# Optimization experiments

Hardware: AMD Instinct MI355X
Metric: run time of the kernel (lower is better)

The kernel has to match this reference:

```python
import jax, jax.numpy as jnp
import numpy as np
from jax import lax

FEAT = 56  # features_size
SR = 2     # sr_ratio
NUM_HEADS = 8

# Constant relative-distance indices, shape (N, N, 2) with values in [0, 2*FEAT-2]
_idx = np.array([[i, j] for i in range(FEAT) for j in range(FEAT)])
REL = jnp.asarray(_idx[None, :, :] - _idx[:, None, :] + FEAT - 1)  # (N, N, 2)


def setup_inputs() -> dict:
    key = jax.random.key(0)
    ks = jax.random.split(key, 8)
    dim = 256
    B = 4
    x = jax.random.normal(ks[0], (B, dim, FEAT, FEAT), dtype=jnp.float32)
    Wq = jax.random.normal(ks[1], (dim, dim), dtype=jnp.float32) * 0.02
    Wkv = jax.random.normal(ks[2], (dim, 2 * dim), dtype=jnp.float32) * 0.02
    sr_w = jax.random.normal(ks[3], (dim, dim, SR, SR), dtype=jnp.float32) * 0.02  # OIHW
    sr_b = jnp.zeros((dim,), dtype=jnp.float32)
    ln_g = jnp.ones((dim,), dtype=jnp.float32)
    ln_b = jnp.zeros((dim,), dtype=jnp.float32)
    pos_emb = jax.random.normal(ks[4], (2 * FEAT - 1, 2 * FEAT - 1), dtype=jnp.float32) * 0.2
    proj_w = jax.random.normal(ks[5], (dim, dim), dtype=jnp.float32) * 0.02
    proj_b = jnp.zeros((dim,), dtype=jnp.float32)
    return {"x": x, "Wq": Wq, "Wkv": Wkv, "sr_w": sr_w, "sr_b": sr_b,
            "ln_g": ln_g, "ln_b": ln_b, "pos_emb": pos_emb,
            "proj_w": proj_w, "proj_b": proj_b}


def reference(x, Wq, Wkv, sr_w, sr_b, ln_g, ln_b, pos_emb, proj_w, proj_b):
    B, C, H, W = x.shape
    N = H * W
    h = NUM_HEADS
    hd = C // h
    scale = hd ** -0.5

    x_q = x.reshape(B, C, N).transpose(0, 2, 1)            # (B, N, C)
    q = (x_q @ Wq).reshape(B, N, h, hd).transpose(0, 2, 1, 3)  # (B, h, N, hd)

    # spatial reduction conv (kernel=stride=SR) + layernorm
    xr = lax.conv_general_dilated(x, sr_w, (SR, SR), 'VALID',
                                  dimension_numbers=('NCHW', 'OIHW', 'NCHW'))
    xr = xr + sr_b[None, :, None, None]
    Nk = (H // SR) * (W // SR)
    x_kv = xr.reshape(B, C, Nk).transpose(0, 2, 1)          # (B, Nk, C)
    mu = jnp.mean(x_kv, axis=-1, keepdims=True)
    var = jnp.var(x_kv, axis=-1, keepdims=True)
    x_kv = (x_kv - mu) * lax.rsqrt(var + 1e-5) * ln_g + ln_b

    # kv projection; einops '(dim h l)' split: head_dim slowest, l fastest
    kv = (x_kv @ Wkv).reshape(B, Nk, hd, h, 2)
    k = kv[..., 0].transpose(0, 3, 1, 2)                    # (B, h, Nk, hd)
    v = kv[..., 1].transpose(0, 3, 1, 2)                    # (B, h, Nk, hd)

    attn = jnp.einsum('bhnd,bhmd->bhnm', q, k) * scale      # (B, h, N, Nk)
    bias = pos_emb[REL[..., 0], REL[..., 1]][:, :Nk]        # (N, Nk)
    attn = jax.nn.softmax(attn + bias, axis=-1)

    out = jnp.einsum('bhnm,bhmd->bhnd', attn, v)            # (B, h, N, hd)
    out = out.transpose(0, 2, 1, 3).reshape(B, N, C)
    out = out @ proj_w + proj_b
    return out.transpose(0, 2, 1).reshape(B, C, H, W)
```

## Files before the change

kernel.cpp:

```cpp
#include <hip/hip_runtime.h>
#include <hip/hip_bf16.h>

typedef float f32x4 __attribute__((ext_vector_type(4)));
typedef short s16x8 __attribute__((ext_vector_type(8)));
typedef unsigned short u16x8 __attribute__((ext_vector_type(8)));

#define MFMA16(a,b,c) __builtin_amdgcn_mfma_f32_16x16x32_bf16(a,b,c,0,0,0)

#define NTOK 3136
#define NKV  784
#define NKVP 800
#define CD   256
#define NH   8
#define HD   32
#define PEW  111
#define LOG2E 1.4426950408889634f
#define SC2  (0.17677669529663687f * 1.4426950408889634f)

static __device__ __forceinline__ unsigned short f2b(float f){
  unsigned int u = __float_as_uint(f);
  return (unsigned short)((u + 0x7fffu + ((u>>16)&1u)) >> 16);
}
static __device__ __forceinline__ unsigned short f2b_fast(float f){
  __hip_bfloat16 h = __float2bfloat16(f);
  return *reinterpret_cast<unsigned short*>(&h);
}
static __device__ __forceinline__ float b2f(unsigned short u){
  return __uint_as_float(((unsigned int)u)<<16);
}

__global__ void k_prepw(const float* __restrict__ Wq, const float* __restrict__ Wkv,
                        const float* __restrict__ pw, const float* __restrict__ srw,
                        unsigned short* __restrict__ WqT, unsigned short* __restrict__ WkvT,
                        unsigned short* __restrict__ pwT, unsigned short* __restrict__ srwb2){
  int i = blockIdx.x*256 + threadIdx.x;
  if (i < 65536){ int nn=i>>8, kk=i&255; WqT[i] = f2b(Wq[kk*256+nn]); }
  else if (i < 196608){ int j=i-65536; int c2=j>>8, kk=j&255; WkvT[j] = f2b(Wkv[kk*512+c2]); }
  else if (i < 262144){ int j=i-196608; int cc=j>>8, kk=j&255; pwT[j] = f2b(pw[kk*256+cc]); }
  else { int j=i-262144; int o=j>>10, rem=j&1023, khw=rem>>8, ci=rem&255;
         srwb2[j] = f2b(srw[o*1024 + ci*4 + khw]); }
}

__global__ void k_bias(const float* __restrict__ pos, unsigned short* __restrict__ bias2){
  int key = blockIdx.x*256 + threadIdx.x;
  int n = blockIdx.y;
  if (key >= NKVP) return;
  float v;
  if (key < NKV){
    int nr = (n*9363)>>19, nc = n - nr*56;
    int tt = (key*9363)>>19, mm = key - tt*56;
    v = pos[(tt-nr+55)*PEW + (mm-nc+55)] * LOG2E;
  } else v = -100000.f;
  bias2[(size_t)n*NKVP + key] = f2b(v);
}

__global__ void k_pad(unsigned short* __restrict__ kb, unsigned short* __restrict__ vT){
  int i = blockIdx.x*256 + threadIdx.x;
  if (i < 16384){
    int bh=i>>9, r=i&511, ridx=r>>5, d=r&31;
    int row = 776 + (ridx&7) + (ridx>>3)*16;
    kb[((size_t)bh*NKVP + row)*HD + d] = 0;
  } else {
    int j=i-16384;
    int bh=j>>9, r=j&511, d=r>>4, key=784+(r&15);
    vT[((size_t)bh*HD + d)*NKVP + key] = 0;
  }
}

__global__ __launch_bounds__(256) void k_xt(const float* __restrict__ x,
                                            unsigned short* __restrict__ xbf){
  __shared__ float tile[64][65];
  const int t = threadIdx.x;
  const int n0 = blockIdx.x*64, c0 = blockIdx.y*64, b = blockIdx.z;
  const int tx = t&15, ty = t>>4;
#pragma unroll
  for (int j=0;j<4;++j){
    f32x4 v = *(const f32x4*)&x[(size_t)(b*CD + c0+ty+j*16)*NTOK + n0 + tx*4];
    tile[ty+j*16][tx*4+0]=v[0]; tile[ty+j*16][tx*4+1]=v[1];
    tile[ty+j*16][tx*4+2]=v[2]; tile[ty+j*16][tx*4+3]=v[3];
  }
  __syncthreads();
  const int nr = t>>2, ccb = (t&3)*16;
  u16x8 o0, o1;
#pragma unroll
  for (int u=0;u<8;++u){ o0[u] = f2b(tile[ccb+u][nr]); o1[u] = f2b(tile[ccb+8+u][nr]); }
  unsigned short* dst = &xbf[((size_t)b*NTOK + n0+nr)*CD + c0 + ccb];
  *(u16x8*)dst = o0;
  *(u16x8*)(dst+8) = o1;
}

__global__ __launch_bounds__(256) void k_qproj(const unsigned short* __restrict__ xbf,
      const unsigned short* __restrict__ WqT, unsigned short* __restrict__ qb){
  const int tid=threadIdx.x, wv=tid>>6, l=tid&63, g=l>>4, ln16=l&15;
  const int bI = blockIdx.x/49;
  const int n0 = (blockIdx.x%49)*64;
  const int m0 = n0 + (wv>>1)*32;
  const int c0 = blockIdx.y*64 + (wv&1)*32;
  const unsigned short* ap0 = &xbf[((size_t)bI*NTOK + m0+ln16)*CD + g*8];
  const unsigned short* ap1 = ap0 + 16*CD;
  const unsigned short* bp0 = &WqT[(size_t)(c0+ln16)*CD + g*8];
  const unsigned short* bp1 = bp0 + 16*CD;
  f32x4 acc[2][2] = {};
  s16x8 a0 = *(const s16x8*)ap0, a1 = *(const s16x8*)ap1;
  s16x8 w0 = *(const s16x8*)bp0, w1 = *(const s16x8*)bp1;
#pragma unroll
  for (int k0=0; k0<CD; k0+=32){
    s16x8 na0 = *(const s16x8*)(ap0 + k0+32);
    s16x8 na1 = *(const s16x8*)(ap1 + k0+32);
    s16x8 nw0 = *(const s16x8*)(bp0 + k0+32);
    s16x8 nw1 = *(const s16x8*)(bp1 + k0+32);
    acc[0][0] = MFMA16(a0, w0, acc[0][0]);
    acc[0][1] = MFMA16(a0, w1, acc[0][1]);
    acc[1][0] = MFMA16(a1, w0, acc[1][0]);
    acc[1][1] = MFMA16(a1, w1, acc[1][1]);
    a0=na0; a1=na1; w0=nw0; w1=nw1;
  }
#pragma unroll
  for (int mi=0;mi<2;++mi)
#pragma unroll
    for (int ni=0;ni<2;++ni){
      int c = c0 + ni*16 + ln16;
#pragma unroll
      for (int r=0;r<4;++r){
        int n = m0 + mi*16 + g*4 + r;
        qb[((size_t)bI*NTOK + n)*CD + c] = f2b(acc[mi][ni][r] * SC2);
      }
    }
}

__global__ __launch_bounds__(256) void k_conv(const unsigned short* __restrict__ xbf,
      const unsigned short* __restrict__ srwb2, const float* __restrict__ srb,
      float* __restrict__ convo){
  const int tid=threadIdx.x, wv=tid>>6, l=tid&63, g=l>>4, ln16=l&15;
  const int m0 = blockIdx.x*64 + (wv>>1)*32;
  const int c0 = blockIdx.y*64 + (wv&1)*32;
  size_t abase[2][4];
#pragma unroll
  for (int mi=0;mi<2;++mi){
    int m = m0 + mi*16 + ln16;
    int bb = (m>=2352)?3:(m>=1568)?2:(m>=784)?1:0;
    int nk = m - bb*784;
    int pp = (nk*9363)>>18, qq = nk - pp*28;
#pragma unroll
    for (int khw=0;khw<4;++khw){
      int kh = khw>>1, kw = khw&1;
      abase[mi][khw] = ((size_t)bb*NTOK + (2*pp+kh)*56 + 2*qq+kw)*CD;
    }
  }
  const unsigned short* wp0 = &srwb2[(size_t)(c0+ln16)*1024 + g*8];
  const unsigned short* wp1 = wp0 + 16*1024;
  f32x4 acc[2][2] = {};
  s16x8 a0 = *(const s16x8*)&xbf[abase[0][0] + g*8];
  s16x8 a1 = *(const s16x8*)&xbf[abase[1][0] + g*8];
  s16x8 w0 = *(const s16x8*)wp0;
  s16x8 w1 = *(const s16x8*)wp1;
#pragma unroll
  for (int s=0; s<32; ++s){
    const int s1 = s+1;
    const int khw2 = (s1>>3)&3, kc2 = (s1&7)*32;
    const int woff = (s1&31)*32;
    s16x8 na0 = *(const s16x8*)&xbf[abase[0][khw2] + kc2 + g*8];
    s16x8 na1 = *(const s16x8*)&xbf[abase[1][khw2] + kc2 + g*8];
    s16x8 nw0 = *(const s16x8*)(wp0 + woff);
    s16x8 nw1 = *(const s16x8*)(wp1 + woff);
    acc[0][0] = MFMA16(a0, w0, acc[0][0]);
    acc[0][1] = MFMA16(a0, w1, acc[0][1]);
    acc[1][0] = MFMA16(a1, w0, acc[1][0]);
    acc[1][1] = MFMA16(a1, w1, acc[1][1]);
    a0=na0; a1=na1; w0=nw0; w1=nw1;
  }
#pragma unroll
  for (int mi=0;mi<2;++mi)
#pragma unroll
    for (int ni=0;ni<2;++ni){
      int c = c0 + ni*16 + ln16;
      float bias = srb[c];
#pragma unroll
      for (int r=0;r<4;++r){
        int m = m0 + mi*16 + g*4 + r;
        convo[(size_t)m*CD + c] = acc[mi][ni][r] + bias;
      }
    }
}

__global__ void k_ln(const float* __restrict__ co, const float* __restrict__ gam,
                     const float* __restrict__ bet, unsigned short* __restrict__ kvbf){
  const int row = blockIdx.x, t = threadIdx.x;
  float v = co[(size_t)row*CD + t];
  float s = v, s2 = v*v;
#pragma unroll
  for (int o=32; o>0; o>>=1){ s += __shfl_down(s,o); s2 += __shfl_down(s2,o); }
  __shared__ float ps[4], ps2[4];
  int wid = t>>6, lane = t&63;
  if (lane==0){ ps[wid]=s; ps2[wid]=s2; }
  __syncthreads();
  if (t==0){
    float a = ps[0]+ps[1]+ps[2]+ps[3];
    float a2 = ps2[0]+ps2[1]+ps2[2]+ps2[3];
    float mu = a*(1.f/CD);
    float var = a2*(1.f/CD) - mu*mu;
    ps[0] = mu; ps2[0] = rsqrtf(var + 1e-5f);
  }
  __syncthreads();
  float mu = ps[0], rs = ps2[0];
  kvbf[(size_t)row*CD + t] = f2b((v-mu)*rs*gam[t] + bet[t]);
}

__global__ __launch_bounds__(256) void k_kv(const unsigned short* __restrict__ kvbf,
      const unsigned short* __restrict__ WkvT, unsigned short* __restrict__ kb,
      unsigned short* __restrict__ vT){
  const int tid=threadIdx.x, wv=tid>>6, l=tid&63, g=l>>4, ln16=l&15;
  const int m0 = blockIdx.x*64 + (wv>>1)*32;
  const int c0 = blockIdx.y*64 + (wv&1)*32;
  const unsigned short* ap0 = &kvbf[(size_t)(m0+ln16)*CD + g*8];
  const unsigned short* ap1 = ap0 + 16*CD;
  const unsigned short* bp0 = &WkvT[(size_t)(c0+ln16)*CD + g*8];
  const unsigned short* bp1 = bp0 + 16*CD;
  f32x4 acc[2][2] = {};
  s16x8 a0 = *(const s16x8*)ap0, a1 = *(const s16x8*)ap1;
  s16x8 w0 = *(const s16x8*)bp0, w1 = *(const s16x8*)bp1;
#pragma unroll
  for (int k0=0; k0<CD; k0+=32){
    s16x8 na0 = *(const s16x8*)(ap0 + k0+32);
    s16x8 na1 = *(const s16x8*)(ap1 + k0+32);
    s16x8 nw0 = *(const s16x8*)(bp0 + k0+32);
    s16x8 nw1 = *(const s16x8*)(bp1 + k0+32);
    acc[0][0] = MFMA16(a0, w0, acc[0][0]);
    acc[0][1] = MFMA16(a0, w1, acc[0][1]);
    acc[1][0] = MFMA16(a1, w0, acc[1][0]);
    acc[1][1] = MFMA16(a1, w1, acc[1][1]);
    a0=na0; a1=na1; w0=nw0; w1=nw1;
  }
#pragma unroll
  for (int mi=0;mi<2;++mi)
#pragma unroll
    for (int ni=0;ni<2;++ni){
      int c2 = c0 + ni*16 + ln16;
      int d = c2>>4, hh = (c2>>1)&7;
#pragma unroll
      for (int r=0;r<4;++r){
        int m = m0 + mi*16 + g*4 + r;
        int bq = (m>=2352)?3:(m>=1568)?2:(m>=784)?1:0;
        int nk = m - bq*784;
        unsigned short val = f2b(acc[mi][ni][r]);
        if (c2&1){
          vT[(((size_t)bq*NH+hh)*HD + d)*NKVP + nk] = val;
        } else {
          int chunk = nk & ~31, pos = nk & 31;
          int gg = pos>>3, jj = pos&7;
          int row = (jj<4) ? (gg*4+jj) : (16 + gg*4 + (jj-4));
          kb[(((size_t)bq*NH+hh)*NKVP + chunk + row)*HD + d] = val;
        }
      }
    }
}

__global__ __launch_bounds__(256) void k_attn(const unsigned short* __restrict__ qb,
      const unsigned short* __restrict__ kb, const unsigned short* __restrict__ vT,
      const unsigned short* __restrict__ bias2, unsigned short* __restrict__ aout){
  const int tid=threadIdx.x, wv=tid>>6, l=tid&63, g=l>>4, ln16=l&15;
  const int bh = blockIdx.y, b = bh>>3, h = bh&7;
  const int nw = blockIdx.x*64 + wv*16;
  const s16x8 qf = *(const s16x8*)&qb[((size_t)b*NTOK + nw + ln16)*CD + h*HD + g*8];
  const unsigned short* kptr  = kb + (size_t)bh*NKVP*HD + ln16*HD + g*8;
  const unsigned short* vptr0 = vT + (size_t)bh*HD*NKVP + ln16*NKVP + g*8;
  const unsigned short* vptr1 = vptr0 + 16*NKVP;
  const unsigned short* bp = bias2 + (size_t)(nw + ln16)*NKVP + g*8;
  f32x4 accO0 = {}, accO1 = {};
  float S = 0.f;
  const f32x4 zf = {};
  s16x8 ka0 = *(const s16x8*)(kptr);
  s16x8 ka1 = *(const s16x8*)(kptr + 16*HD);
  s16x8 v0  = *(const s16x8*)(vptr0);
  s16x8 v1  = *(const s16x8*)(vptr1);
  u16x8 bb  = *(const u16x8*)(bp);
#pragma unroll 5
  for (int it=0; it<25; ++it){
    kptr += 32*HD; vptr0 += 32; vptr1 += 32; bp += 32;
    s16x8 nk0 = *(const s16x8*)(kptr);
    s16x8 nk1 = *(const s16x8*)(kptr + 16*HD);
    s16x8 nv0 = *(const s16x8*)(vptr0);
    s16x8 nv1 = *(const s16x8*)(vptr1);
    u16x8 nbb = *(const u16x8*)(bp);
    f32x4 d0 = MFMA16(ka0, qf, zf);
    f32x4 d1 = MFMA16(ka1, qf, zf);
    float p[8];
#pragma unroll
    for (int r=0;r<4;++r){
      p[r]   = exp2f(d0[r] + b2f(bb[r]));
      p[4+r] = exp2f(d1[r] + b2f(bb[4+r]));
    }
    S += ((p[0]+p[1])+(p[2]+p[3])) + ((p[4]+p[5])+(p[6]+p[7]));
    s16x8 pf;
#pragma unroll
    for (int j=0;j<8;++j) pf[j] = (short)f2b_fast(p[j]);
    accO0 = MFMA16(pf, v0, accO0);
    accO1 = MFMA16(pf, v1, accO1);
    ka0=nk0; ka1=nk1; v0=nv0; v1=nv1; bb=nbb;
  }
  S += __shfl_xor(S, 16);
  S += __shfl_xor(S, 32);
#pragma unroll
  for (int r=0;r<4;++r){
    float Sr = __shfl(S, g*4 + r);
    float inv = 1.f / Sr;
    int n = nw + g*4 + r;
    aout[((size_t)b*NTOK + n)*CD + h*HD + ln16]      = f2b(accO0[r]*inv);
    aout[((size_t)b*NTOK + n)*CD + h*HD + 16 + ln16] = f2b(accO1[r]*inv);
  }
}

__global__ __launch_bounds__(256) void k_proj(const unsigned short* __restrict__ ain,
      const unsigned short* __restrict__ pwT, const float* __restrict__ pb,
      float* __restrict__ out){
  const int tid=threadIdx.x, wv=tid>>6, l=tid&63, g=l>>4, ln16=l&15;
  const int bI = blockIdx.x/49;
  const int n0 = (blockIdx.x%49)*64;
  const int nsub = n0 + (wv&1)*32;
  const int c0 = blockIdx.y*64 + (wv>>1)*32;
  const unsigned short* ap0 = &pwT[(size_t)(c0+ln16)*CD + g*8];
  const unsigned short* ap1 = ap0 + 16*CD;
  const unsigned short* bp0 = &ain[((size_t)bI*NTOK + nsub+ln16)*CD + g*8];
  const unsigned short* bp1 = bp0 + 16*CD;
  f32x4 acc[2][2] = {};
  s16x8 a0 = *(const s16x8*)ap0, a1 = *(const s16x8*)ap1;
  s16x8 w0 = *(const s16x8*)bp0, w1 = *(const s16x8*)bp1;
#pragma unroll
  for (int k0=0; k0<CD; k0+=32){
    s16x8 na0 = *(const s16x8*)(ap0 + k0+32);
    s16x8 na1 = *(const s16x8*)(ap1 + k0+32);
    s16x8 nw0 = *(const s16x8*)(bp0 + k0+32);
    s16x8 nw1 = *(const s16x8*)(bp1 + k0+32);
    acc[0][0] = MFMA16(a0, w0, acc[0][0]);
    acc[0][1] = MFMA16(a0, w1, acc[0][1]);
    acc[1][0] = MFMA16(a1, w0, acc[1][0]);
    acc[1][1] = MFMA16(a1, w1, acc[1][1]);
    a0=na0; a1=na1; w0=nw0; w1=nw1;
  }
#pragma unroll
  for (int mi=0;mi<2;++mi)
#pragma unroll
    for (int r=0;r<4;++r){
      int c = c0 + mi*16 + g*4 + r;
      float bias = pb[c];
#pragma unroll
      for (int ni=0;ni<2;++ni){
        int n = nsub + ni*16 + ln16;
        out[((size_t)bI*CD + c)*NTOK + n] = acc[mi][ni][r] + bias;
      }
    }
}

extern "C" void kernel_launch(void* const* d_in, const int* in_sizes, int n_in,
                              void* d_out, int out_size, void* d_ws, size_t ws_size,
                              hipStream_t stream){
  const float* x   = (const float*)d_in[0];
  const float* Wq  = (const float*)d_in[1];
  const float* Wkv = (const float*)d_in[2];
  const float* srw = (const float*)d_in[3];
  const float* srb = (const float*)d_in[4];
  const float* lng = (const float*)d_in[5];
  const float* lnb = (const float*)d_in[6];
  const float* pos = (const float*)d_in[7];
  const float* pw  = (const float*)d_in[8];
  const float* pb  = (const float*)d_in[9];
  float* out = (float*)d_out;

  unsigned char* p = (unsigned char*)d_ws;
  unsigned short* WqT   = (unsigned short*)(p + 0);
  unsigned short* WkvT  = (unsigned short*)(p + 131072);
  unsigned short* pwT   = (unsigned short*)(p + 393216);
  unsigned short* srwb2 = (unsigned short*)(p + 524288);
  unsigned short* bias2 = (unsigned short*)(p + 1048576);
  unsigned short* xbf   = (unsigned short*)(p + 6066176);
  unsigned short* qbuf  = (unsigned short*)(p + 12488704);
  float*          convo = (float*)        (p + 18911232);
  unsigned short* kvbf  = (unsigned short*)(p + 22122496);
  unsigned short* kbuf  = (unsigned short*)(p + 23728128);
  unsigned short* vT    = (unsigned short*)(p + 25366528);
  unsigned short* aout  = (unsigned short*)(p + 27004928);

  k_prepw<<<2048, 256, 0, stream>>>(Wq, Wkv, pw, srw, WqT, WkvT, pwT, srwb2);
  k_bias <<<dim3(4,3136), 256, 0, stream>>>(pos, bias2);
  k_pad  <<<128, 256, 0, stream>>>(kbuf, vT);
  k_xt   <<<dim3(49,4,4), 256, 0, stream>>>(x, xbf);
  k_qproj<<<dim3(196,4), 256, 0, stream>>>(xbf, WqT, qbuf);
  k_conv <<<dim3(49,4),  256, 0, stream>>>(xbf, srwb2, srb, convo);
  k_ln   <<<3136, 256, 0, stream>>>(convo, lng, lnb, kvbf);
  k_kv   <<<dim3(49,8),  256, 0, stream>>>(kvbf, WkvT, kbuf, vT);
  k_attn <<<dim3(49,32), 256, 0, stream>>>(qbuf, kbuf, vT, bias2, aout);
  k_proj <<<dim3(196,4), 256, 0, stream>>>(aout, pwT, pb, out);
}
```

Baseline: 220.1 us.

## Stage K/V tiles through LDS with async loads and merge prep kernels

The four preprocessing kernels (weight transpose, bias table, padding, x transpose) are merged into one launch, and the bias table is now written as 4-element vectors per thread. The attention kernel now has the whole block share K and V tiles: they are loaded once per block into double-buffered LDS with global_load_lds, instead of each wave loading its own copy from global memory. The grid is also swapped so blocks of the same batch-head run next to each other, which should improve L2 reuse. This cuts redundant global K/V traffic and launch overhead, but adds a __syncthreads per iteration and an LDS read stage.

```diff
diff --git a/kernel.cpp b/kernel.cpp
--- a/kernel.cpp
+++ b/kernel.cpp
@@ -3,6 +3,7 @@
 
 typedef float f32x4 __attribute__((ext_vector_type(4)));
 typedef short s16x8 __attribute__((ext_vector_type(8)));
+typedef unsigned short u16x4 __attribute__((ext_vector_type(4)));
 typedef unsigned short u16x8 __attribute__((ext_vector_type(8)));
 
 #define MFMA16(a,b,c) __builtin_amdgcn_mfma_f32_16x16x32_bf16(a,b,c,0,0,0)
@@ -28,65 +29,77 @@
 static __device__ __forceinline__ float b2f(unsigned short u){
   return __uint_as_float(((unsigned int)u)<<16);
 }
-
-__global__ void k_prepw(const float* __restrict__ Wq, const float* __restrict__ Wkv,
-                        const float* __restrict__ pw, const float* __restrict__ srw,
-                        unsigned short* __restrict__ WqT, unsigned short* __restrict__ WkvT,
-                        unsigned short* __restrict__ pwT, unsigned short* __restrict__ srwb2){
-  int i = blockIdx.x*256 + threadIdx.x;
-  if (i < 65536){ int nn=i>>8, kk=i&255; WqT[i] = f2b(Wq[kk*256+nn]); }
-  else if (i < 196608){ int j=i-65536; int c2=j>>8, kk=j&255; WkvT[j] = f2b(Wkv[kk*512+c2]); }
-  else if (i < 262144){ int j=i-196608; int cc=j>>8, kk=j&255; pwT[j] = f2b(pw[kk*256+cc]); }
-  else { int j=i-262144; int o=j>>10, rem=j&1023, khw=rem>>8, ci=rem&255;
-         srwb2[j] = f2b(srw[o*1024 + ci*4 + khw]); }
-}
-
-__global__ void k_bias(const float* __restrict__ pos, unsigned short* __restrict__ bias2){
-  int key = blockIdx.x*256 + threadIdx.x;
-  int n = blockIdx.y;
-  if (key >= NKVP) return;
-  float v;
-  if (key < NKV){
-    int nr = (n*9363)>>19, nc = n - nr*56;
-    int tt = (key*9363)>>19, mm = key - tt*56;
-    v = pos[(tt-nr+55)*PEW + (mm-nc+55)] * LOG2E;
-  } else v = -100000.f;
-  bias2[(size_t)n*NKVP + key] = f2b(v);
-}
-
-__global__ void k_pad(unsigned short* __restrict__ kb, unsigned short* __restrict__ vT){
-  int i = blockIdx.x*256 + threadIdx.x;
-  if (i < 16384){
-    int bh=i>>9, r=i&511, ridx=r>>5, d=r&31;
-    int row = 776 + (ridx&7) + (ridx>>3)*16;
-    kb[((size_t)bh*NKVP + row)*HD + d] = 0;
+static __device__ __forceinline__ void gload16(const unsigned short* g, unsigned short* l){
+  __builtin_amdgcn_global_load_lds(
+      (const __attribute__((address_space(1))) unsigned int*)g,
+      (__attribute__((address_space(3))) unsigned int*)l, 16, 0, 0);
+}
+
+__global__ __launch_bounds__(256) void k_prep(
+      const float* __restrict__ Wq, const float* __restrict__ Wkv,
+      const float* __restrict__ pw, const float* __restrict__ srw,
+      const float* __restrict__ pos, const float* __restrict__ x,
+      unsigned short* __restrict__ WqT, unsigned short* __restrict__ WkvT,
+      unsigned short* __restrict__ pwT, unsigned short* __restrict__ srwb2,
+      unsigned short* __restrict__ bias2, unsigned short* __restrict__ xbf,
+      unsigned short* __restrict__ kb, unsigned short* __restrict__ vT){
+  __shared__ float tile[64][65];
+  const int blk = blockIdx.x, t = threadIdx.x;
+  if (blk < 2048){
+    int i = blk*256 + t;
+    if (i < 65536){ int nn=i>>8, kk=i&255; WqT[i] = f2b(Wq[kk*256+nn]); }
+    else if (i < 196608){ int j=i-65536; int c2=j>>8, kk=j&255; WkvT[j] = f2b(Wkv[kk*512+c2]); }
+    else if (i < 262144){ int j=i-196608; int cc=j>>8, kk=j&255; pwT[j] = f2b(pw[kk*256+cc]); }
+    else { int j=i-262144; int o=j>>10, rem=j&1023, khw=rem>>8, ci=rem&255;
+           srwb2[j] = f2b(srw[o*1024 + ci*4 + khw]); }
+  } else if (blk < 2176){
+    int i = (blk-2048)*256 + t;
+    if (i < 16384){
+      int bh=i>>9, r=i&511, ridx=r>>5, d=r&31;
+      int row = 776 + (ridx&7) + (ridx>>3)*16;
+      kb[((size_t)bh*NKVP + row)*HD + d] = 0;
+    } else {
+      int j=i-16384;
+      int bh=j>>9, r=j&511, d=r>>4, key=784+(r&15);
+      vT[((size_t)bh*HD + d)*NKVP + key] = 0;
+    }
+  } else if (blk < 5312){
+    int n = blk - 2176;
+    if (t < 200){
+      int nr = (n*9363)>>19, nc = n - nr*56;
+      u16x4 o;
+#pragma unroll
+      for (int j=0;j<4;++j){
+        int key = t*4 + j;
+        float v;
+        if (key < NKV){
+          int tt = (key*9363)>>19, mm = key - tt*56;
+          v = pos[(tt-nr+55)*PEW + (mm-nc+55)] * LOG2E;
+        } else v = -100000.f;
+        o[j] = f2b(v);
+      }
+      *(u16x4*)&bias2[(size_t)n*NKVP + t*4] = o;
+    }
   } else {
-    int j=i-16384;
-    int bh=j>>9, r=j&511, d=r>>4, key=784+(r&15);
-    vT[((size_t)bh*HD + d)*NKVP + key] = 0;
-  }
-}
-
-__global__ __launch_bounds__(256) void k_xt(const float* __restrict__ x,
-                                            unsigned short* __restrict__ xbf){
-  __shared__ float tile[64][65];
-  const int t = threadIdx.x;
-  const int n0 = blockIdx.x*64, c0 = blockIdx.y*64, b = blockIdx.z;
-  const int tx = t&15, ty = t>>4;
-#pragma unroll
-  for (int j=0;j<4;++j){
-    f32x4 v = *(const f32x4*)&x[(size_t)(b*CD + c0+ty+j*16)*NTOK + n0 + tx*4];
-    tile[ty+j*16][tx*4+0]=v[0]; tile[ty+j*16][tx*4+1]=v[1];
-    tile[ty+j*16][tx*4+2]=v[2]; tile[ty+j*16][tx*4+3]=v[3];
-  }
-  __syncthreads();
-  const int nr = t>>2, ccb = (t&3)*16;
-  u16x8 o0, o1;
-#pragma unroll
-  for (int u=0;u<8;++u){ o0[u] = f2b(tile[ccb+u][nr]); o1[u] = f2b(tile[ccb+8+u][nr]); }
-  unsigned short* dst = &xbf[((size_t)b*NTOK + n0+nr)*CD + c0 + ccb];
-  *(u16x8*)dst = o0;
-  *(u16x8*)(dst+8) = o1;
+    int bx = blk - 5312;
+    const int n0 = (bx%49)*64; int c4 = bx/49;
+    const int c0 = (c4&3)*64, b = c4>>2;
+    const int tx = t&15, ty = t>>4;
+#pragma unroll
+    for (int j=0;j<4;++j){
+      f32x4 v = *(const f32x4*)&x[(size_t)(b*CD + c0+ty+j*16)*NTOK + n0 + tx*4];
+      tile[ty+j*16][tx*4+0]=v[0]; tile[ty+j*16][tx*4+1]=v[1];
+      tile[ty+j*16][tx*4+2]=v[2]; tile[ty+j*16][tx*4+3]=v[3];
+    }
+    __syncthreads();
+    const int nr = t>>2, ccb = (t&3)*16;
+    u16x8 o0, o1;
+#pragma unroll
+    for (int u=0;u<8;++u){ o0[u] = f2b(tile[ccb+u][nr]); o1[u] = f2b(tile[ccb+8+u][nr]); }
+    unsigned short* dst = &xbf[((size_t)b*NTOK + n0+nr)*CD + c0 + ccb];
+    *(u16x8*)dst = o0;
+    *(u16x8*)(dst+8) = o1;
+  }
 }
 
 __global__ __launch_bounds__(256) void k_qproj(const unsigned short* __restrict__ xbf,
@@ -258,30 +271,39 @@
 __global__ __launch_bounds__(256) void k_attn(const unsigned short* __restrict__ qb,
       const unsigned short* __restrict__ kb, const unsigned short* __restrict__ vT,
       const unsigned short* __restrict__ bias2, unsigned short* __restrict__ aout){
+  __shared__ unsigned short kv[2][2048];
   const int tid=threadIdx.x, wv=tid>>6, l=tid&63, g=l>>4, ln16=l&15;
-  const int bh = blockIdx.y, b = bh>>3, h = bh&7;
-  const int nw = blockIdx.x*64 + wv*16;
+  const int bh = blockIdx.x, b = bh>>3, h = bh&7;
+  const int nw = blockIdx.y*64 + wv*16;
   const s16x8 qf = *(const s16x8*)&qb[((size_t)b*NTOK + nw + ln16)*CD + h*HD + g*8];
-  const unsigned short* kptr  = kb + (size_t)bh*NKVP*HD + ln16*HD + g*8;
-  const unsigned short* vptr0 = vT + (size_t)bh*HD*NKVP + ln16*NKVP + g*8;
-  const unsigned short* vptr1 = vptr0 + 16*NKVP;
+  const unsigned short* kbase = kb + (size_t)bh*NKVP*HD;
+  const unsigned short* vbase = vT + (size_t)bh*HD*NKVP;
   const unsigned short* bp = bias2 + (size_t)(nw + ln16)*NKVP + g*8;
+  const unsigned short* sp = (wv < 2)
+      ? (kbase + wv*512 + l*8)
+      : (vbase + (size_t)((wv&1)*16 + (l>>2))*NKVP + (l&3)*8);
+  const int sstep = (wv < 2) ? 1024 : 32;
+  unsigned short* ldst0 = &kv[0][wv*512];
+  unsigned short* ldst1 = &kv[1][wv*512];
   f32x4 accO0 = {}, accO1 = {};
   float S = 0.f;
   const f32x4 zf = {};
-  s16x8 ka0 = *(const s16x8*)(kptr);
-  s16x8 ka1 = *(const s16x8*)(kptr + 16*HD);
-  s16x8 v0  = *(const s16x8*)(vptr0);
-  s16x8 v1  = *(const s16x8*)(vptr1);
-  u16x8 bb  = *(const u16x8*)(bp);
-#pragma unroll 5
+  gload16(sp, ldst0);
+  u16x8 bb = *(const u16x8*)bp;
+  __syncthreads();
+  int cur = 0;
   for (int it=0; it<25; ++it){
-    kptr += 32*HD; vptr0 += 32; vptr1 += 32; bp += 32;
-    s16x8 nk0 = *(const s16x8*)(kptr);
-    s16x8 nk1 = *(const s16x8*)(kptr + 16*HD);
-    s16x8 nv0 = *(const s16x8*)(vptr0);
-    s16x8 nv1 = *(const s16x8*)(vptr1);
-    u16x8 nbb = *(const u16x8*)(bp);
+    u16x8 nbb = bb;
+    if (it < 24){
+      gload16(sp + (it+1)*sstep, cur ? ldst0 : ldst1);
+      nbb = *(const u16x8*)(bp + (it+1)*32);
+    }
+    __builtin_amdgcn_sched_barrier(0);
+    const unsigned short* kc = kv[cur];
+    s16x8 ka0 = *(const s16x8*)&kc[ln16*32 + g*8];
+    s16x8 ka1 = *(const s16x8*)&kc[512 + ln16*32 + g*8];
+    s16x8 v0  = *(const s16x8*)&kc[1024 + ln16*32 + g*8];
+    s16x8 v1  = *(const s16x8*)&kc[1536 + ln16*32 + g*8];
     f32x4 d0 = MFMA16(ka0, qf, zf);
     f32x4 d1 = MFMA16(ka1, qf, zf);
     float p[8];
@@ -296,7 +318,8 @@
     for (int j=0;j<8;++j) pf[j] = (short)f2b_fast(p[j]);
     accO0 = MFMA16(pf, v0, accO0);
     accO1 = MFMA16(pf, v1, accO1);
-    ka0=nk0; ka1=nk1; v0=nv0; v1=nv1; bb=nbb;
+    __syncthreads();
+    cur ^= 1; bb = nbb;
   }
   S += __shfl_xor(S, 16);
   S += __shfl_xor(S, 32);
@@ -380,14 +403,12 @@
   unsigned short* vT    = (unsigned short*)(p + 25366528);
   unsigned short* aout  = (unsigned short*)(p + 27004928);
 
-  k_prepw<<<2048, 256, 0, stream>>>(Wq, Wkv, pw, srw, WqT, WkvT, pwT, srwb2);
-  k_bias <<<dim3(4,3136), 256, 0, stream>>>(pos, bias2);
-  k_pad  <<<128, 256, 0, stream>>>(kbuf, vT);
-  k_xt   <<<dim3(49,4,4), 256, 0, stream>>>(x, xbf);
+  k_prep <<<6096, 256, 0, stream>>>(Wq, Wkv, pw, srw, pos, x,
+                                    WqT, WkvT, pwT, srwb2, bias2, xbf, kbuf, vT);
   k_qproj<<<dim3(196,4), 256, 0, stream>>>(xbf, WqT, qbuf);
   k_conv <<<dim3(49,4),  256, 0, stream>>>(xbf, srwb2, srb, convo);
   k_ln   <<<3136, 256, 0, stream>>>(convo, lng, lnb, kvbf);
   k_kv   <<<dim3(49,8),  256, 0, stream>>>(kvbf, WkvT, kbuf, vT);
-  k_attn <<<dim3(49,32), 256, 0, stream>>>(qbuf, kbuf, vT, bias2, aout);
+  k_attn <<<dim3(32,49), 256, 0, stream>>>(qbuf, kbuf, vT, bias2, aout);
   k_proj <<<dim3(196,4), 256, 0, stream>>>(aout, pwT, pb, out);
 }
```

New measurement: 198.2 us. 1.11x faster.
